# Performance work log

Measured on AMD Instinct MI355X. Metric: run time of the kernel, lower is better.

The kernel has to match this reference:

```python
import jax, jax.numpy as jnp
import numpy as np

NUM_WIRES = 18
NUM_LAYERS = 3
BATCH = 64
DIM = 2 ** NUM_WIRES


def _apply_ry(psi, theta, w):
    # RY(t) = [[cos(t/2), -sin(t/2)], [sin(t/2), cos(t/2)]] on wire w (wire 0 = MSB)
    B = psi.shape[0]
    c = jnp.cos(theta * 0.5).astype(psi.dtype)
    s = jnp.sin(theta * 0.5).astype(psi.dtype)
    p = psi.reshape(B, 2 ** w, 2, -1)
    a, b = p[:, :, 0], p[:, :, 1]
    return jnp.stack([c * a - s * b, s * a + c * b], axis=2).reshape(B, -1)


def _apply_rz(psi, theta, w):
    # RZ(t) = diag(e^{-i t/2}, e^{+i t/2}) on wire w
    B = psi.shape[0]
    half = (theta * 0.5).astype(jnp.complex64)
    p0 = jnp.exp(-1j * half)
    p1 = jnp.exp(1j * half)
    p = psi.reshape(B, 2 ** w, 2, -1)
    return jnp.stack([p0 * p[:, :, 0], p1 * p[:, :, 1]], axis=2).reshape(B, -1)


def _apply_cnot_adjacent(psi, w):
    # CNOT with control w, target w+1: flip target bit where control bit = 1
    B = psi.shape[0]
    p = psi.reshape(B, 2 ** w, 2, 2, -1)
    p = p.at[:, :, 1].set(p[:, :, 1, ::-1])
    return p.reshape(B, -1)


def _expval_z(psi, w):
    # <Z_w> = P(bit_w = 0) - P(bit_w = 1)
    B = psi.shape[0]
    prob = (psi.real ** 2 + psi.imag ** 2).reshape(B, 2 ** w, 2, -1)
    p = prob.sum(axis=(1, 3))  # (B, 2)
    return p[:, 0] - p[:, 1]


def _circuit(psi, params):
    for layer in range(params.shape[0]):
        for w in range(NUM_WIRES):
            psi = _apply_ry(psi, params[layer, 0, w], w)
            psi = _apply_rz(psi, params[layer, 1, w], w)
        for w in range(NUM_WIRES - 1):
            psi = _apply_cnot_adjacent(psi, w)
    # expvals of PauliZ on every wire -> (B, num_wires)
    return jnp.stack([_expval_z(psi, w) for w in range(NUM_WIRES)], axis=-1)


def setup_inputs() -> dict:
    key = jax.random.key(0)
    k1, k2, k3, k4, k5 = jax.random.split(key, 5)
    state_re = jax.random.normal(k1, (BATCH, DIM), dtype=jnp.float32)
    state_im = jax.random.normal(k2, (BATCH, DIM), dtype=jnp.float32)
    norm = jnp.sqrt(jnp.sum(state_re ** 2 + state_im ** 2, axis=-1, keepdims=True))
    state_re = state_re / norm
    state_im = state_im / norm
    params = jax.random.normal(k3, (NUM_LAYERS, 2, NUM_WIRES), dtype=jnp.float32)
    head_w = jax.random.normal(k4, (1, NUM_WIRES), dtype=jnp.float32) / np.sqrt(NUM_WIRES)
    head_b = jax.random.normal(k5, (1,), dtype=jnp.float32) / np.sqrt(NUM_WIRES)
    return {"state_re": state_re, "state_im": state_im, "params": params,
            "head_w": head_w, "head_b": head_b}


def reference(state_re, state_im, params, head_w, head_b):
    psi = (state_re + 1j * state_im).astype(jnp.complex64)  # (B, 2^n)
    feats = _circuit(psi, params)                            # (B, n)
    out = feats @ head_w.T + head_b                          # (B, 1)
    return out[:, 0]
```

## Files before the change

### kernel.cpp

```cpp
#include <hip/hip_runtime.h>


#define LROW 36u
#define LDSW 2304u

static __device__ __forceinline__ float rfl(float x) {
    return __int_as_float(__builtin_amdgcn_readfirstlane(__float_as_int(x)));
}

template<int J>
__device__ __forceinline__ void sqg(float* ar, float* ai, float c, float s, float pc, float ps) {
#pragma unroll
    for (int r = 0; r < 32; ++r) {
        if (((r >> J) & 1) == 0) {
            const int r1 = r + (1 << J);
            const float a0r = ar[r], a0i = ai[r], a1r = ar[r1], a1i = ai[r1];
            ar[r] = fmaf(c, a0r, -(s * a1r));
            ai[r] = fmaf(c, a0i, -(s * a1i));
            const float t1r = fmaf(s, a0r, c * a1r);
            const float t1i = fmaf(s, a0i, c * a1i);
            ar[r1] = fmaf(pc, t1r, -(ps * t1i));
            ai[r1] = fmaf(pc, t1i,  (ps * t1r));
        }
    }
}

__global__ __launch_bounds__(128) void passB_k(float* __restrict__ re, float* __restrict__ im,
                                               const float* __restrict__ params, int layer)
{
    __shared__ float lds[2 * LDSW];
    const int t   = threadIdx.x;
    const int l   = t & 63;
    const int wib = t >> 6;
    float* Lb = lds + wib * LDSW;
    const int wv  = (blockIdx.x << 1) | wib;
    const int b   = wv >> 7;
    const int mid = wv & 127;
    const int L5 = (l >> 5) & 1, L4 = (l >> 4) & 1, L3 = (l >> 3) & 1, L2 = (l >> 2) & 1;
    const int L1 = (l >> 1) & 1, L0 = l & 1;

    const unsigned base = ((unsigned)b << 18) | ((unsigned)mid << 4);
    const unsigned sel  = (L5 << 17) | (L4 << 16) | (L3 << 12) | (L2 << 11) | (L1 << 3) | (L0 << 2);

    float C[7], S[7], PC[7], PS[7];
    const float* pl = params + layer * 36;
#pragma unroll
    for (int k = 0; k < 7; ++k) {
        const int w = 6 - k;
        float sv, cv;
        __sincosf(0.5f * pl[w], &sv, &cv);  S[k] = rfl(sv);  C[k] = rfl(cv);
        __sincosf(pl[18 + w], &sv, &cv);    PS[k] = rfl(sv); PC[k] = rfl(cv);
    }

    float ar[32], ai[32];
#pragma unroll
    for (int g = 0; g < 8; ++g) {
        const unsigned n = base + sel + ((unsigned)g << 13);
        const float4 vr = *(const float4*)&re[n];
        const float4 vi = *(const float4*)&im[n];
        ar[4*g+0] = vr.x; ar[4*g+1] = vr.y; ar[4*g+2] = vr.z; ar[4*g+3] = vr.w;
        ai[4*g+0] = vi.x; ai[4*g+1] = vi.y; ai[4*g+2] = vi.z; ai[4*g+3] = vi.w;
    }

    sqg<4>(ar, ai, C[4], S[4], PC[4], PS[4]);
    sqg<3>(ar, ai, C[3], S[3], PC[3], PS[3]);
    sqg<2>(ar, ai, C[2], S[2], PC[2], PS[2]);

    const unsigned tb = (unsigned)L0 * 144u + (unsigned)(l >> 1);
#pragma unroll
    for (int g = 0; g < 8; ++g)
#pragma unroll
        for (int c = 0; c < 4; ++c)
            Lb[tb + g * 288 + c * 36] = ar[4*g+c];
#pragma unroll
    for (int q = 0; q < 8; ++q) {
        const float4 v = *(const float4*)&Lb[(unsigned)l * LROW + (q << 2)];
        ar[4*q+0] = v.x; ar[4*q+1] = v.y; ar[4*q+2] = v.z; ar[4*q+3] = v.w;
    }
#pragma unroll
    for (int g = 0; g < 8; ++g)
#pragma unroll
        for (int c = 0; c < 4; ++c)
            Lb[tb + g * 288 + c * 36] = ai[4*g+c];
#pragma unroll
    for (int q = 0; q < 8; ++q) {
        const float4 v = *(const float4*)&Lb[(unsigned)l * LROW + (q << 2)];
        ai[4*q+0] = v.x; ai[4*q+1] = v.y; ai[4*q+2] = v.z; ai[4*q+3] = v.w;
    }

    sqg<4>(ar, ai, C[6], S[6], PC[6], PS[6]);
    sqg<3>(ar, ai, C[5], S[5], PC[5], PS[5]);
    sqg<2>(ar, ai, C[1], S[1], PC[1], PS[1]);
    sqg<1>(ar, ai, C[0], S[0], PC[0], PS[0]);

#pragma unroll
    for (int q = 0; q < 8; ++q)
        *(float4*)&Lb[(unsigned)l * LROW + (q << 2)] =
            make_float4(ar[4*q+0], ar[4*q+1], ar[4*q+2], ar[4*q+3]);
#pragma unroll
    for (int g = 0; g < 8; ++g)
#pragma unroll
        for (int c = 0; c < 4; ++c)
            ar[4*g+c] = Lb[tb + g * 288 + c * 36];
#pragma unroll
    for (int q = 0; q < 8; ++q)
        *(float4*)&Lb[(unsigned)l * LROW + (q << 2)] =
            make_float4(ai[4*q+0], ai[4*q+1], ai[4*q+2], ai[4*q+3]);
#pragma unroll
    for (int g = 0; g < 8; ++g)
#pragma unroll
        for (int c = 0; c < 4; ++c)
            ai[4*g+c] = Lb[tb + g * 288 + c * 36];

#pragma unroll
    for (int g = 0; g < 8; ++g) {
        int h = (L5 << 6) | (L4 << 5) | (g << 2) | (L3 << 1) | L2;
        int x = h ^ (h >> 1); x ^= x >> 2; x ^= x >> 4;
        const unsigned n = base + ((unsigned)x << 11) + (L1 << 3) + (L0 << 2);
        *(float4*)&re[n] = make_float4(ar[4*g+0], ar[4*g+1], ar[4*g+2], ar[4*g+3]);
        *(float4*)&im[n] = make_float4(ai[4*g+0], ai[4*g+1], ai[4*g+2], ai[4*g+3]);
    }
}

template<bool FINAL>
__global__ __launch_bounds__(128) void passA_k(float* __restrict__ re, float* __restrict__ im,
                                               const float* __restrict__ params, int layer,
                                               const float* __restrict__ hw,
                                               const float* __restrict__ hb,
                                               float* __restrict__ out)
{
    __shared__ float lds[2 * LDSW];
    const int t   = threadIdx.x;
    const int l   = t & 63;
    const int wib = t >> 6;
    float* Lb = lds + wib * LDSW;
    const int wv  = (blockIdx.x << 1) | wib;
    const int b   = wv >> 7;
    const int hi7 = wv & 127;
    const int n11 = hi7 & 1;
    const unsigned base = ((unsigned)b << 18) | ((unsigned)hi7 << 11);

    float C[11], S[11], PC[11], PS[11];
    const float* pl = params + layer * 36;
#pragma unroll
    for (int k = 0; k < 11; ++k) {
        const int w = 17 - k;
        float sv, cv;
        __sincosf(0.5f * pl[w], &sv, &cv);  S[k] = rfl(sv);  C[k] = rfl(cv);
        __sincosf(pl[18 + w], &sv, &cv);    PS[k] = rfl(sv); PC[k] = rfl(cv);
    }

    float ar[32], ai[32];
#pragma unroll
    for (int g = 0; g < 8; ++g) {
        const unsigned n = base + ((unsigned)g << 8) + ((unsigned)l << 2);
        const float4 vr = *(const float4*)&re[n];
        const float4 vi = *(const float4*)&im[n];
        ar[4*g+0] = vr.x; ar[4*g+1] = vr.y; ar[4*g+2] = vr.z; ar[4*g+3] = vr.w;
        ai[4*g+0] = vi.x; ai[4*g+1] = vi.y; ai[4*g+2] = vi.z; ai[4*g+3] = vi.w;
    }

    sqg<4>(ar, ai, C[10], S[10], PC[10], PS[10]);
    sqg<3>(ar, ai, C[9],  S[9],  PC[9],  PS[9]);
    sqg<2>(ar, ai, C[8],  S[8],  PC[8],  PS[8]);
    sqg<1>(ar, ai, C[1],  S[1],  PC[1],  PS[1]);
    sqg<0>(ar, ai, C[0],  S[0],  PC[0],  PS[0]);

    {
        const int side   = (l >> 5) & 1;
        const float c7   = C[7];
        const float bco  = side ? S[7] : -S[7];
        const float qc   = side ? PC[7] : 1.f;
        const float qs   = side ? PS[7] : 0.f;
#pragma unroll
        for (int r = 0; r < 32; ++r) {
            const float pr = __shfl_xor(ar[r], 32);
            const float pi = __shfl_xor(ai[r], 32);
            const float tr = fmaf(c7, ar[r], bco * pr);
            const float ti = fmaf(c7, ai[r], bco * pi);
            ar[r] = fmaf(qc, tr, -(qs * ti));
            ai[r] = fmaf(qc, ti,  (qs * tr));
        }
    }

    const unsigned tb = (unsigned)((l >> 5) & 1) * 144u + (unsigned)(l & 31);
#pragma unroll
    for (int g = 0; g < 8; ++g)
#pragma unroll
        for (int c = 0; c < 4; ++c)
            Lb[tb + g * 288 + c * 36] = ar[4*g+c];
#pragma unroll
    for (int q = 0; q < 8; ++q) {
        const float4 v = *(const float4*)&Lb[(unsigned)l * LROW + (q << 2)];
        ar[4*q+0] = v.x; ar[4*q+1] = v.y; ar[4*q+2] = v.z; ar[4*q+3] = v.w;
    }
#pragma unroll
    for (int g = 0; g < 8; ++g)
#pragma unroll
        for (int c = 0; c < 4; ++c)
            Lb[tb + g * 288 + c * 36] = ai[4*g+c];
#pragma unroll
    for (int q = 0; q < 8; ++q) {
        const float4 v = *(const float4*)&Lb[(unsigned)l * LROW + (q << 2)];
        ai[4*q+0] = v.x; ai[4*q+1] = v.y; ai[4*q+2] = v.z; ai[4*q+3] = v.w;
    }

    sqg<4>(ar, ai, C[6], S[6], PC[6], PS[6]);
    sqg<3>(ar, ai, C[5], S[5], PC[5], PS[5]);
    sqg<2>(ar, ai, C[4], S[4], PC[4], PS[4]);
    sqg<1>(ar, ai, C[3], S[3], PC[3], PS[3]);
    sqg<0>(ar, ai, C[2], S[2], PC[2], PS[2]);

#pragma unroll
    for (int q = 0; q < 8; ++q)
        *(float4*)&Lb[(unsigned)l * LROW + (q << 2)] =
            make_float4(ar[4*q+0], ar[4*q+1], ar[4*q+2], ar[4*q+3]);
#pragma unroll
    for (int g = 0; g < 8; ++g)
#pragma unroll
        for (int c = 0; c < 4; ++c)
            ar[4*g+c] = Lb[tb + g * 288 + c * 36];
#pragma unroll
    for (int q = 0; q < 8; ++q)
        *(float4*)&Lb[(unsigned)l * LROW + (q << 2)] =
            make_float4(ai[4*q+0], ai[4*q+1], ai[4*q+2], ai[4*q+3]);
#pragma unroll
    for (int g = 0; g < 8; ++g)
#pragma unroll
        for (int c = 0; c < 4; ++c)
            ai[4*g+c] = Lb[tb + g * 288 + c * 36];

    const int msk = n11 ? 0x1FF : 0;

    if (!FINAL) {
#pragma unroll
        for (int g = 0; g < 8; ++g) {
            int h = (g << 6) | l;
            int x = h ^ (h >> 1); x ^= x >> 2; x ^= x >> 4; x ^= x >> 8;
            x ^= msk;
            const int y = x & 1;
            const float r0 = ar[4*g+0], r1 = ar[4*g+1], r2 = ar[4*g+2], r3 = ar[4*g+3];
            const float i0 = ai[4*g+0], i1 = ai[4*g+1], i2 = ai[4*g+2], i3 = ai[4*g+3];
            float4 sr, si;
            sr.x = y ? r2 : r0;  sr.y = y ? r3 : r1;  sr.z = y ? r1 : r3;  sr.w = y ? r0 : r2;
            si.x = y ? i2 : i0;  si.y = y ? i3 : i1;  si.z = y ? i1 : i3;  si.w = y ? i0 : i2;
            const unsigned n = base + ((unsigned)x << 2);
            *(float4*)&re[n] = sr;
            *(float4*)&im[n] = si;
        }
    } else {
        float Ghi = 0.f;
#pragma unroll
        for (int j = 0; j < 7; ++j) {
            const float wv_ = hw[6 - j];
            Ghi += ((hi7 >> j) & 1) ? -wv_ : wv_;
        }
        float acc = 0.f;
#pragma unroll
        for (int g = 0; g < 8; ++g) {
            int h = (g << 6) | l;
            int x = h ^ (h >> 1); x ^= x >> 2; x ^= x >> 4; x ^= x >> 8;
            x ^= msk;
            const float q0 = fmaf(ar[4*g+0], ar[4*g+0], ai[4*g+0] * ai[4*g+0]);
            const float q1 = fmaf(ar[4*g+1], ar[4*g+1], ai[4*g+1] * ai[4*g+1]);
            const float q2 = fmaf(ar[4*g+2], ar[4*g+2], ai[4*g+2] * ai[4*g+2]);
            const float q3 = fmaf(ar[4*g+3], ar[4*g+3], ai[4*g+3] * ai[4*g+3]);
            const float psum = (q0 + q1) + (q2 + q3);
            const float d1   = (q0 + q1) - (q2 + q3);
            const float d0   = (q0 - q1) - (q2 - q3);
            float Gm = 0.f;
#pragma unroll
            for (int j = 0; j < 9; ++j) {
                const float wv_ = hw[15 - j];
                Gm += ((x >> j) & 1) ? -wv_ : wv_;
            }
            const float ys = (x & 1) ? -1.f : 1.f;
            acc += psum * (Ghi + Gm) + ys * fmaf(d1, hw[16], d0 * hw[17]);
        }
        if (hi7 == 0 && l == 0) acc += hb[0];
#pragma unroll
        for (int off = 32; off > 0; off >>= 1) acc += __shfl_xor(acc, off);
        if (l == 0) atomicAdd(&out[b], acc);
    }
}

extern "C" void kernel_launch(void* const* d_in, const int* in_sizes, int n_in,
                              void* d_out, int out_size, void* d_ws, size_t ws_size,
                              hipStream_t stream)
{
    float* re           = (float*)d_in[0];
    float* im           = (float*)d_in[1];
    const float* params = (const float*)d_in[2];
    const float* hw     = (const float*)d_in[3];
    const float* hb     = (const float*)d_in[4];
    float* out          = (float*)d_out;
    (void)in_sizes; (void)n_in; (void)d_ws; (void)ws_size;

    hipMemsetAsync(out, 0, (size_t)out_size * sizeof(float), stream);

    const dim3 grid(4096), blk(128);
    for (int l = 0; l < 3; ++l) {
        passB_k<<<grid, blk, 0, stream>>>(re, im, params, l);
        if (l < 2) passA_k<false><<<grid, blk, 0, stream>>>(re, im, params, l, nullptr, nullptr, nullptr);
        else       passA_k<true ><<<grid, blk, 0, stream>>>(re, im, params, l, hw, hb, out);
    }
}
```

Measured before the change: 458.7 us.

## Store intermediate statevector as packed bf16 complex and ping-pong between input buffers

Between passes the statevector is stored as one 32-bit word per amplitude, holding bf16 real and imaginary parts, instead of two fp32 arrays. This roughly halves global memory traffic for the intermediate passes. The first passB skips its gray-code write permutation and folds it into the following passA read address. passA now issues its loads before computing coefficients and fuses the two lowest-wire gates into the unpack loop. The cost is bf16 rounding error at every pass, which may exceed tolerance against a complex64 reference, and the input buffers are overwritten.

```diff
diff --git a/kernel.cpp b/kernel.cpp
--- a/kernel.cpp
+++ b/kernel.cpp
@@ -6,6 +6,27 @@
 
 static __device__ __forceinline__ float rfl(float x) {
     return __int_as_float(__builtin_amdgcn_readfirstlane(__float_as_int(x)));
+}
+
+static __device__ __forceinline__ void unpack2(unsigned u, float& re, float& im) {
+    re = __uint_as_float(u << 16);
+    im = __uint_as_float(u & 0xFFFF0000u);
+}
+static __device__ __forceinline__ unsigned packbf(float a, float b) {
+    unsigned ua = __float_as_uint(a); ua += 0x7FFFu + ((ua >> 16) & 1u);
+    unsigned ub = __float_as_uint(b); ub += 0x7FFFu + ((ub >> 16) & 1u);
+    return (ua >> 16) | (ub & 0xFFFF0000u);
+}
+
+static __device__ __forceinline__ void sq_pair(float& a0r, float& a0i, float& a1r, float& a1i,
+                                               float c, float s, float pc, float ps) {
+    const float t0r = fmaf(c, a0r, -(s * a1r));
+    const float t0i = fmaf(c, a0i, -(s * a1i));
+    const float t1r = fmaf(s, a0r,  c * a1r);
+    const float t1i = fmaf(s, a0i,  c * a1i);
+    a0r = t0r; a0i = t0i;
+    a1r = fmaf(pc, t1r, -(ps * t1i));
+    a1i = fmaf(pc, t1i,  (ps * t1r));
 }
 
 template<int J>
@@ -14,26 +35,86 @@
     for (int r = 0; r < 32; ++r) {
         if (((r >> J) & 1) == 0) {
             const int r1 = r + (1 << J);
-            const float a0r = ar[r], a0i = ai[r], a1r = ar[r1], a1i = ai[r1];
-            ar[r] = fmaf(c, a0r, -(s * a1r));
-            ai[r] = fmaf(c, a0i, -(s * a1i));
-            const float t1r = fmaf(s, a0r, c * a1r);
-            const float t1i = fmaf(s, a0i, c * a1i);
-            ar[r1] = fmaf(pc, t1r, -(ps * t1i));
-            ai[r1] = fmaf(pc, t1i,  (ps * t1r));
-        }
-    }
-}
-
-__global__ __launch_bounds__(128) void passB_k(float* __restrict__ re, float* __restrict__ im,
-                                               const float* __restrict__ params, int layer)
+            sq_pair(ar[r], ai[r], ar[r1], ai[r1], c, s, pc, ps);
+        }
+    }
+}
+
+struct BCoef { float C[7], S[7], PC[7], PS[7]; };
+
+static __device__ __forceinline__ void passB_body(float* ar, float* ai, float* Lb,
+                                                  const BCoef& k, int l) {
+    const int L0 = l & 1;
+    sqg<4>(ar, ai, k.C[4], k.S[4], k.PC[4], k.PS[4]);
+    sqg<3>(ar, ai, k.C[3], k.S[3], k.PC[3], k.PS[3]);
+    sqg<2>(ar, ai, k.C[2], k.S[2], k.PC[2], k.PS[2]);
+
+    const unsigned tb = (unsigned)L0 * 144u + (unsigned)(l >> 1);
+#pragma unroll
+    for (int g = 0; g < 8; ++g)
+#pragma unroll
+        for (int c = 0; c < 4; ++c)
+            Lb[tb + g * 288 + c * 36] = ar[4*g+c];
+#pragma unroll
+    for (int q = 0; q < 8; ++q) {
+        const float4 v = *(const float4*)&Lb[(unsigned)l * LROW + (q << 2)];
+        ar[4*q+0] = v.x; ar[4*q+1] = v.y; ar[4*q+2] = v.z; ar[4*q+3] = v.w;
+    }
+#pragma unroll
+    for (int g = 0; g < 8; ++g)
+#pragma unroll
+        for (int c = 0; c < 4; ++c)
+            Lb[tb + g * 288 + c * 36] = ai[4*g+c];
+#pragma unroll
+    for (int q = 0; q < 8; ++q) {
+        const float4 v = *(const float4*)&Lb[(unsigned)l * LROW + (q << 2)];
+        ai[4*q+0] = v.x; ai[4*q+1] = v.y; ai[4*q+2] = v.z; ai[4*q+3] = v.w;
+    }
+
+    sqg<4>(ar, ai, k.C[6], k.S[6], k.PC[6], k.PS[6]);
+    sqg<3>(ar, ai, k.C[5], k.S[5], k.PC[5], k.PS[5]);
+    sqg<2>(ar, ai, k.C[1], k.S[1], k.PC[1], k.PS[1]);
+    sqg<1>(ar, ai, k.C[0], k.S[0], k.PC[0], k.PS[0]);
+
+#pragma unroll
+    for (int q = 0; q < 8; ++q)
+        *(float4*)&Lb[(unsigned)l * LROW + (q << 2)] =
+            make_float4(ar[4*q+0], ar[4*q+1], ar[4*q+2], ar[4*q+3]);
+#pragma unroll
+    for (int g = 0; g < 8; ++g)
+#pragma unroll
+        for (int c = 0; c < 4; ++c)
+            ar[4*g+c] = Lb[tb + g * 288 + c * 36];
+#pragma unroll
+    for (int q = 0; q < 8; ++q)
+        *(float4*)&Lb[(unsigned)l * LROW + (q << 2)] =
+            make_float4(ai[4*q+0], ai[4*q+1], ai[4*q+2], ai[4*q+3]);
+#pragma unroll
+    for (int g = 0; g < 8; ++g)
+#pragma unroll
+        for (int c = 0; c < 4; ++c)
+            ai[4*g+c] = Lb[tb + g * 288 + c * 36];
+}
+
+static __device__ __forceinline__ void passB_coefs(BCoef& k, const float* pl) {
+#pragma unroll
+    for (int j = 0; j < 7; ++j) {
+        const int w = 6 - j;
+        float sv, cv;
+        __sincosf(0.5f * pl[w], &sv, &cv);  k.S[j] = rfl(sv);  k.C[j] = rfl(cv);
+        __sincosf(pl[18 + w], &sv, &cv);    k.PS[j] = rfl(sv); k.PC[j] = rfl(cv);
+    }
+}
+
+__global__ __launch_bounds__(128) void passB1_k(const float* re, const float* im,
+                                                unsigned* u, const float* __restrict__ params)
 {
     __shared__ float lds[2 * LDSW];
     const int t   = threadIdx.x;
     const int l   = t & 63;
     const int wib = t >> 6;
     float* Lb = lds + wib * LDSW;
-    const int wv  = (blockIdx.x << 1) | wib;
+    const int wv  = ((int)blockIdx.x << 1) | wib;
     const int b   = wv >> 7;
     const int mid = wv & 127;
     const int L5 = (l >> 5) & 1, L4 = (l >> 4) & 1, L3 = (l >> 3) & 1, L2 = (l >> 2) & 1;
@@ -41,16 +122,6 @@
 
     const unsigned base = ((unsigned)b << 18) | ((unsigned)mid << 4);
     const unsigned sel  = (L5 << 17) | (L4 << 16) | (L3 << 12) | (L2 << 11) | (L1 << 3) | (L0 << 2);
-
-    float C[7], S[7], PC[7], PS[7];
-    const float* pl = params + layer * 36;
-#pragma unroll
-    for (int k = 0; k < 7; ++k) {
-        const int w = 6 - k;
-        float sv, cv;
-        __sincosf(0.5f * pl[w], &sv, &cv);  S[k] = rfl(sv);  C[k] = rfl(cv);
-        __sincosf(pl[18 + w], &sv, &cv);    PS[k] = rfl(sv); PC[k] = rfl(cv);
-    }
 
     float ar[32], ai[32];
 #pragma unroll
@@ -62,68 +133,71 @@
         ai[4*g+0] = vi.x; ai[4*g+1] = vi.y; ai[4*g+2] = vi.z; ai[4*g+3] = vi.w;
     }
 
-    sqg<4>(ar, ai, C[4], S[4], PC[4], PS[4]);
-    sqg<3>(ar, ai, C[3], S[3], PC[3], PS[3]);
-    sqg<2>(ar, ai, C[2], S[2], PC[2], PS[2]);
-
-    const unsigned tb = (unsigned)L0 * 144u + (unsigned)(l >> 1);
-#pragma unroll
-    for (int g = 0; g < 8; ++g)
-#pragma unroll
-        for (int c = 0; c < 4; ++c)
-            Lb[tb + g * 288 + c * 36] = ar[4*g+c];
-#pragma unroll
-    for (int q = 0; q < 8; ++q) {
-        const float4 v = *(const float4*)&Lb[(unsigned)l * LROW + (q << 2)];
-        ar[4*q+0] = v.x; ar[4*q+1] = v.y; ar[4*q+2] = v.z; ar[4*q+3] = v.w;
-    }
-#pragma unroll
-    for (int g = 0; g < 8; ++g)
-#pragma unroll
-        for (int c = 0; c < 4; ++c)
-            Lb[tb + g * 288 + c * 36] = ai[4*g+c];
-#pragma unroll
-    for (int q = 0; q < 8; ++q) {
-        const float4 v = *(const float4*)&Lb[(unsigned)l * LROW + (q << 2)];
-        ai[4*q+0] = v.x; ai[4*q+1] = v.y; ai[4*q+2] = v.z; ai[4*q+3] = v.w;
-    }
-
-    sqg<4>(ar, ai, C[6], S[6], PC[6], PS[6]);
-    sqg<3>(ar, ai, C[5], S[5], PC[5], PS[5]);
-    sqg<2>(ar, ai, C[1], S[1], PC[1], PS[1]);
-    sqg<1>(ar, ai, C[0], S[0], PC[0], PS[0]);
-
-#pragma unroll
-    for (int q = 0; q < 8; ++q)
-        *(float4*)&Lb[(unsigned)l * LROW + (q << 2)] =
-            make_float4(ar[4*q+0], ar[4*q+1], ar[4*q+2], ar[4*q+3]);
-#pragma unroll
-    for (int g = 0; g < 8; ++g)
-#pragma unroll
-        for (int c = 0; c < 4; ++c)
-            ar[4*g+c] = Lb[tb + g * 288 + c * 36];
-#pragma unroll
-    for (int q = 0; q < 8; ++q)
-        *(float4*)&Lb[(unsigned)l * LROW + (q << 2)] =
-            make_float4(ai[4*q+0], ai[4*q+1], ai[4*q+2], ai[4*q+3]);
-#pragma unroll
-    for (int g = 0; g < 8; ++g)
-#pragma unroll
-        for (int c = 0; c < 4; ++c)
-            ai[4*g+c] = Lb[tb + g * 288 + c * 36];
+    BCoef k; passB_coefs(k, params);
+    passB_body(ar, ai, Lb, k, l);
+
+#pragma unroll
+    for (int g = 0; g < 8; ++g) {
+        const int h = (L5 << 6) | (L4 << 5) | (g << 2) | (L3 << 1) | L2;
+        const unsigned n = base + ((unsigned)h << 11) + (L1 << 3) + (L0 << 2);
+        uint4 pv;
+        pv.x = packbf(ar[4*g+0], ai[4*g+0]);
+        pv.y = packbf(ar[4*g+1], ai[4*g+1]);
+        pv.z = packbf(ar[4*g+2], ai[4*g+2]);
+        pv.w = packbf(ar[4*g+3], ai[4*g+3]);
+        *(uint4*)&u[n] = pv;
+    }
+}
+
+__global__ __launch_bounds__(128) void passBk_k(const unsigned* __restrict__ src,
+                                                unsigned* __restrict__ dst,
+                                                const float* __restrict__ params, int layer)
+{
+    __shared__ float lds[2 * LDSW];
+    const int t   = threadIdx.x;
+    const int l   = t & 63;
+    const int wib = t >> 6;
+    float* Lb = lds + wib * LDSW;
+    const int wv  = ((int)blockIdx.x << 1) | wib;
+    const int b   = wv >> 7;
+    const int mid = wv & 127;
+    const int L5 = (l >> 5) & 1, L4 = (l >> 4) & 1, L3 = (l >> 3) & 1, L2 = (l >> 2) & 1;
+    const int L1 = (l >> 1) & 1, L0 = l & 1;
+
+    const unsigned base = ((unsigned)b << 18) | ((unsigned)mid << 4);
+    const unsigned sel  = (L5 << 17) | (L4 << 16) | (L3 << 12) | (L2 << 11) | (L1 << 3) | (L0 << 2);
+
+    float ar[32], ai[32];
+#pragma unroll
+    for (int g = 0; g < 8; ++g) {
+        const unsigned n = base + sel + ((unsigned)g << 13);
+        const uint4 pv = *(const uint4*)&src[n];
+        unpack2(pv.x, ar[4*g+0], ai[4*g+0]);
+        unpack2(pv.y, ar[4*g+1], ai[4*g+1]);
+        unpack2(pv.z, ar[4*g+2], ai[4*g+2]);
+        unpack2(pv.w, ar[4*g+3], ai[4*g+3]);
+    }
+
+    BCoef k; passB_coefs(k, params + layer * 36);
+    passB_body(ar, ai, Lb, k, l);
 
 #pragma unroll
     for (int g = 0; g < 8; ++g) {
         int h = (L5 << 6) | (L4 << 5) | (g << 2) | (L3 << 1) | L2;
         int x = h ^ (h >> 1); x ^= x >> 2; x ^= x >> 4;
         const unsigned n = base + ((unsigned)x << 11) + (L1 << 3) + (L0 << 2);
-        *(float4*)&re[n] = make_float4(ar[4*g+0], ar[4*g+1], ar[4*g+2], ar[4*g+3]);
-        *(float4*)&im[n] = make_float4(ai[4*g+0], ai[4*g+1], ai[4*g+2], ai[4*g+3]);
-    }
-}
-
-template<bool FINAL>
-__global__ __launch_bounds__(128) void passA_k(float* __restrict__ re, float* __restrict__ im,
+        uint4 pv;
+        pv.x = packbf(ar[4*g+0], ai[4*g+0]);
+        pv.y = packbf(ar[4*g+1], ai[4*g+1]);
+        pv.z = packbf(ar[4*g+2], ai[4*g+2]);
+        pv.w = packbf(ar[4*g+3], ai[4*g+3]);
+        *(uint4*)&dst[n] = pv;
+    }
+}
+
+template<bool FIRST, bool FINAL>
+__global__ __launch_bounds__(128) void passA_k(const unsigned* __restrict__ src,
+                                               unsigned* __restrict__ dst,
                                                const float* __restrict__ params, int layer,
                                                const float* __restrict__ hw,
                                                const float* __restrict__ hb,
@@ -134,37 +208,45 @@
     const int l   = t & 63;
     const int wib = t >> 6;
     float* Lb = lds + wib * LDSW;
-    const int wv  = (blockIdx.x << 1) | wib;
+    const int wv  = ((int)blockIdx.x << 1) | wib;
     const int b   = wv >> 7;
-    const int hi7 = wv & 127;
-    const int n11 = hi7 & 1;
-    const unsigned base = ((unsigned)b << 18) | ((unsigned)hi7 << 11);
+    const int L   = wv & 127;
+    const int hip = FIRST ? (L ^ (L >> 1)) : L;
+    const int n11 = L & 1;
+    const unsigned baseL = ((unsigned)b << 18) | ((unsigned)hip << 11);
+    const unsigned baseS = ((unsigned)b << 18) | ((unsigned)L << 11);
+
+    uint4 U[8];
+#pragma unroll
+    for (int g = 0; g < 8; ++g)
+        U[g] = *(const uint4*)&src[baseL + ((unsigned)g << 8) + ((unsigned)l << 2)];
 
     float C[11], S[11], PC[11], PS[11];
     const float* pl = params + layer * 36;
 #pragma unroll
-    for (int k = 0; k < 11; ++k) {
-        const int w = 17 - k;
+    for (int p = 0; p < 11; ++p) {
+        const int w = 17 - p;
         float sv, cv;
-        __sincosf(0.5f * pl[w], &sv, &cv);  S[k] = rfl(sv);  C[k] = rfl(cv);
-        __sincosf(pl[18 + w], &sv, &cv);    PS[k] = rfl(sv); PC[k] = rfl(cv);
+        __sincosf(0.5f * pl[w], &sv, &cv);  S[p] = rfl(sv);  C[p] = rfl(cv);
+        __sincosf(pl[18 + w], &sv, &cv);    PS[p] = rfl(sv); PC[p] = rfl(cv);
     }
 
     float ar[32], ai[32];
 #pragma unroll
     for (int g = 0; g < 8; ++g) {
-        const unsigned n = base + ((unsigned)g << 8) + ((unsigned)l << 2);
-        const float4 vr = *(const float4*)&re[n];
-        const float4 vi = *(const float4*)&im[n];
-        ar[4*g+0] = vr.x; ar[4*g+1] = vr.y; ar[4*g+2] = vr.z; ar[4*g+3] = vr.w;
-        ai[4*g+0] = vi.x; ai[4*g+1] = vi.y; ai[4*g+2] = vi.z; ai[4*g+3] = vi.w;
+        unpack2(U[g].x, ar[4*g+0], ai[4*g+0]);
+        unpack2(U[g].y, ar[4*g+1], ai[4*g+1]);
+        unpack2(U[g].z, ar[4*g+2], ai[4*g+2]);
+        unpack2(U[g].w, ar[4*g+3], ai[4*g+3]);
+        sq_pair(ar[4*g+0], ai[4*g+0], ar[4*g+2], ai[4*g+2], C[1], S[1], PC[1], PS[1]);
+        sq_pair(ar[4*g+1], ai[4*g+1], ar[4*g+3], ai[4*g+3], C[1], S[1], PC[1], PS[1]);
+        sq_pair(ar[4*g+0], ai[4*g+0], ar[4*g+1], ai[4*g+1], C[0], S[0], PC[0], PS[0]);
+        sq_pair(ar[4*g+2], ai[4*g+2], ar[4*g+3], ai[4*g+3], C[0], S[0], PC[0], PS[0]);
     }
 
     sqg<4>(ar, ai, C[10], S[10], PC[10], PS[10]);
     sqg<3>(ar, ai, C[9],  S[9],  PC[9],  PS[9]);
     sqg<2>(ar, ai, C[8],  S[8],  PC[8],  PS[8]);
-    sqg<1>(ar, ai, C[1],  S[1],  PC[1],  PS[1]);
-    sqg<0>(ar, ai, C[0],  S[0],  PC[0],  PS[0]);
 
     {
         const int side   = (l >> 5) & 1;
@@ -241,19 +323,19 @@
             const int y = x & 1;
             const float r0 = ar[4*g+0], r1 = ar[4*g+1], r2 = ar[4*g+2], r3 = ar[4*g+3];
             const float i0 = ai[4*g+0], i1 = ai[4*g+1], i2 = ai[4*g+2], i3 = ai[4*g+3];
-            float4 sr, si;
-            sr.x = y ? r2 : r0;  sr.y = y ? r3 : r1;  sr.z = y ? r1 : r3;  sr.w = y ? r0 : r2;
-            si.x = y ? i2 : i0;  si.y = y ? i3 : i1;  si.z = y ? i1 : i3;  si.w = y ? i0 : i2;
-            const unsigned n = base + ((unsigned)x << 2);
-            *(float4*)&re[n] = sr;
-            *(float4*)&im[n] = si;
+            uint4 pv;
+            pv.x = y ? packbf(r2, i2) : packbf(r0, i0);
+            pv.y = y ? packbf(r3, i3) : packbf(r1, i1);
+            pv.z = y ? packbf(r1, i1) : packbf(r3, i3);
+            pv.w = y ? packbf(r0, i0) : packbf(r2, i2);
+            *(uint4*)&dst[baseS + ((unsigned)x << 2)] = pv;
         }
     } else {
         float Ghi = 0.f;
 #pragma unroll
         for (int j = 0; j < 7; ++j) {
             const float wv_ = hw[6 - j];
-            Ghi += ((hi7 >> j) & 1) ? -wv_ : wv_;
+            Ghi += ((L >> j) & 1) ? -wv_ : wv_;
         }
         float acc = 0.f;
 #pragma unroll
@@ -277,7 +359,7 @@
             const float ys = (x & 1) ? -1.f : 1.f;
             acc += psum * (Ghi + Gm) + ys * fmaf(d1, hw[16], d0 * hw[17]);
         }
-        if (hi7 == 0 && l == 0) acc += hb[0];
+        if (L == 0 && l == 0) acc += hb[0];
 #pragma unroll
         for (int off = 32; off > 0; off >>= 1) acc += __shfl_xor(acc, off);
         if (l == 0) atomicAdd(&out[b], acc);
@@ -288,8 +370,10 @@
                               void* d_out, int out_size, void* d_ws, size_t ws_size,
                               hipStream_t stream)
 {
-    float* re           = (float*)d_in[0];
-    float* im           = (float*)d_in[1];
+    const float* re0    = (const float*)d_in[0];
+    const float* im0    = (const float*)d_in[1];
+    unsigned* u0        = (unsigned*)d_in[0];
+    unsigned* u1        = (unsigned*)d_in[1];
     const float* params = (const float*)d_in[2];
     const float* hw     = (const float*)d_in[3];
     const float* hb     = (const float*)d_in[4];
@@ -299,9 +383,10 @@
     hipMemsetAsync(out, 0, (size_t)out_size * sizeof(float), stream);
 
     const dim3 grid(4096), blk(128);
-    for (int l = 0; l < 3; ++l) {
-        passB_k<<<grid, blk, 0, stream>>>(re, im, params, l);
-        if (l < 2) passA_k<false><<<grid, blk, 0, stream>>>(re, im, params, l, nullptr, nullptr, nullptr);
-        else       passA_k<true ><<<grid, blk, 0, stream>>>(re, im, params, l, hw, hb, out);
-    }
-}
+    passB1_k             <<<grid, blk, 0, stream>>>(re0, im0, u0, params);
+    passA_k<true,  false><<<grid, blk, 0, stream>>>(u0, u1, params, 0, nullptr, nullptr, nullptr);
+    passBk_k             <<<grid, blk, 0, stream>>>(u1, u0, params, 1);
+    passA_k<false, false><<<grid, blk, 0, stream>>>(u0, u1, params, 1, nullptr, nullptr, nullptr);
+    passBk_k             <<<grid, blk, 0, stream>>>(u1, u0, params, 2);
+    passA_k<false, true ><<<grid, blk, 0, stream>>>(u0, nullptr, params, 2, hw, hb, out);
+}
```

New measurement: 396.8 us. 13.5% less time.
